# Optimization experiments

Measured on AMD Instinct MI355X. Metric: run time of the kernel, lower is better.

Reference implementation:

```python
import jax, jax.numpy as jnp
import numpy as np

B, C, H, W = 8, 384, 32, 32
NH, DK, DV = 8, 48, 48
CFF = 4 * C
L = H * W
NBIAS = (2 * H - 1) * (2 * W - 1)
LN_EPS = 1e-5


def _relative_indices(height, width):
    # rel_idx[q, k] = (gy_k - gy_q + H) * W + (gx_k - gx_q + W), matching the torch loop
    gy, gx = np.meshgrid(np.arange(height), np.arange(width), indexing='ij')
    gy = gy.ravel(); gx = gx.ravel()
    rel = (gy[None, :] - gy[:, None] + height) * width + (gx[None, :] - gx[:, None] + width)
    return jnp.asarray(rel, dtype=jnp.int64)


def setup_inputs() -> dict:
    key = jax.random.key(0)
    ks = jax.random.split(key, 10)
    s = 0.02  # small init scale
    return {
        'x': jax.random.normal(ks[0], (B, C, H, W), dtype=jnp.float32),
        'gamma': jnp.ones((C,), jnp.float32),
        'beta': jnp.zeros((C,), jnp.float32),
        'Wq': jax.random.normal(ks[1], (NH * DK, C), jnp.float32) * s,
        'Wk': jax.random.normal(ks[2], (NH * DK, C), jnp.float32) * s,
        'Wv': jax.random.normal(ks[3], (NH * DV, C), jnp.float32) * s,
        'Wo': jax.random.normal(ks[4], (C, NH * DV), jnp.float32) * s,
        'bo': jnp.zeros((C,), jnp.float32),
        'rel_bias': jax.random.normal(ks[5], (NH, NBIAS), jnp.float32),
        'fc1_w': jax.random.normal(ks[6], (CFF, C), jnp.float32) * s,
        'fc1_b': jnp.zeros((CFF,), jnp.float32),
        'fc2_w': jax.random.normal(ks[7], (C, CFF), jnp.float32) * s,
        'fc2_b': jnp.zeros((C,), jnp.float32),
        'rel_idx': _relative_indices(H, W),
    }


def reference(x, gamma, beta, Wq, Wk, Wv, Wo, bo, rel_bias,
              fc1_w, fc1_b, fc2_w, fc2_b, rel_idx):
    b, c, h_sp, w_sp = x.shape
    l = h_sp * w_sp
    nh = rel_bias.shape[0]
    dk = Wq.shape[0] // nh
    dv = Wv.shape[0] // nh

    # LayerNorm over channel dim (NHWC), then flatten to tokens [b, l, c]
    t = jnp.transpose(x, (0, 2, 3, 1))
    mu = jnp.mean(t, axis=-1, keepdims=True)
    var = jnp.mean(jnp.square(t - mu), axis=-1, keepdims=True)
    t = (t - mu) / jnp.sqrt(var + LN_EPS) * gamma + beta
    tok = t.reshape(b, l, c)

    q = (tok @ Wq.T).reshape(b, l, nh, dk)
    k = (tok @ Wk.T).reshape(b, l, nh, dk)
    v = (tok @ Wv.T).reshape(b, l, nh, dv)

    # gathered relative position bias: [nh, l, l]
    bias = rel_bias[:, rel_idx]
    # note: original applies NO 1/sqrt(d_k) scaling
    scores = jnp.einsum('blhd,bmhd->bhlm', q, k) + bias[None]
    attn = jax.nn.softmax(scores, axis=-1)
    out = jnp.einsum('bhlm,bmhd->blhd', attn, v).reshape(b, l, nh * dv)
    out = out @ Wo.T + bo  # [b, l, c]
    out = jnp.transpose(out, (0, 2, 1)).reshape(b, c, h_sp, w_sp)

    y = x + out  # attention residual (x_stem = x, no downsampling)

    # FFN: 1x1 convs == per-pixel linear over channels; exact (erf) gelu as torch default
    u = jnp.einsum('bchw,oc->bohw', y, fc1_w) + fc1_b[None, :, None, None]
    u = jax.nn.gelu(u, approximate=False)
    u = jnp.einsum('bchw,oc->bohw', u, fc2_w) + fc2_b[None, :, None, None]
    return y + u
```

## Files before the change

kernel.cpp:

```cpp
#include <hip/hip_runtime.h>
#include <math.h>

#define SL 1024
#define CH 384
#define NHEAD 8
#define DH 48
#define NBIAS 3969
#define NTOK 8192
#define BATCH 8
#define CFF 1536
#define LN_EPS 1e-5f
#define QKVLD 1152
#define HMS 3145728

#define WQKV_OFF 0
#define WO_OFF   442368
#define F1_OFF   589824
#define F2_OFF   1179648
#define WTOT     1769472

typedef float floatx4 __attribute__((ext_vector_type(4)));
typedef short bf16x8 __attribute__((ext_vector_type(8)));

__device__ __forceinline__ unsigned f2bf_u(float f) {
  unsigned u = __float_as_uint(f);
  return (u + 0x7fffu + ((u >> 16) & 1u)) >> 16;
}
__device__ __forceinline__ unsigned pack2(float a, float b) {
  return f2bf_u(a) | (f2bf_u(b) << 16);
}

__device__ __forceinline__ void gload_lds16(const void* g, void* l) {
  __builtin_amdgcn_global_load_lds(
      (const __attribute__((address_space(1))) void*)g,
      (__attribute__((address_space(3))) void*)l, 16, 0, 0);
}

__global__ void k_w2bf(const float* __restrict__ Wq, const float* __restrict__ Wk,
                       const float* __restrict__ Wv, const float* __restrict__ Wo,
                       const float* __restrict__ f1, const float* __restrict__ f2,
                       short* __restrict__ dst) {
  size_t i = ((size_t)blockIdx.x * 256 + threadIdx.x) * 8;
  if (i >= WTOT) return;
  const float* s;
  size_t base;
  if (i < 147456)        { s = Wq; base = 0; }
  else if (i < 294912)   { s = Wk; base = 147456; }
  else if (i < WO_OFF)   { s = Wv; base = 294912; }
  else if (i < F1_OFF)   { s = Wo; base = WO_OFF; }
  else if (i < F2_OFF)   { s = f1; base = F1_OFF; }
  else                   { s = f2; base = F2_OFF; }
  const float4* p = (const float4*)(s + (i - base));
  float4 a = p[0], b = p[1];
  uint4 o;
  o.x = pack2(a.x, a.y); o.y = pack2(a.z, a.w);
  o.z = pack2(b.x, b.y); o.w = pack2(b.z, b.w);
  *(uint4*)(dst + i) = o;
}

__global__ __launch_bounds__(256) void k_ln_fused(
    const float* __restrict__ x, const float* __restrict__ gamma,
    const float* __restrict__ beta, short* __restrict__ tok) {
  __shared__ float sx[32][385];
  int b = blockIdx.y, l0 = blockIdx.x * 32;
  int tid = threadIdx.x;
  const float* xb = x + (size_t)b * CH * SL;
  int cr = tid >> 3, ls = (tid & 7) * 4;
#pragma unroll
  for (int c0 = 0; c0 < CH; c0 += 32) {
    int c = c0 + cr;
    float4 v = *(const float4*)(xb + (size_t)c * SL + l0 + ls);
    sx[ls + 0][c] = v.x; sx[ls + 1][c] = v.y;
    sx[ls + 2][c] = v.z; sx[ls + 3][c] = v.w;
  }
  __syncthreads();
  int tl = tid >> 3, p = tid & 7;
  float vals[48];
  float s = 0.f, q = 0.f;
#pragma unroll
  for (int i = 0; i < 48; i++) {
    float v = sx[tl][p * 48 + i];
    vals[i] = v; s += v; q += v * v;
  }
  s += __shfl_xor(s, 1, 64); q += __shfl_xor(q, 1, 64);
  s += __shfl_xor(s, 2, 64); q += __shfl_xor(q, 2, 64);
  s += __shfl_xor(s, 4, 64); q += __shfl_xor(q, 4, 64);
  float mu = s * (1.0f / CH);
  float rstd = rsqrtf(q * (1.0f / CH) - mu * mu + LN_EPS);
  short* orow = tok + (size_t)(b * SL + l0 + tl) * CH + p * 48;
#pragma unroll
  for (int i = 0; i < 48; i += 2) {
    float a = (vals[i] - mu) * rstd * gamma[p * 48 + i] + beta[p * 48 + i];
    float c = (vals[i + 1] - mu) * rstd * gamma[p * 48 + i + 1] + beta[p * 48 + i + 1];
    *(unsigned*)(orow + i) = pack2(a, c);
  }
}

template <int BM, bool GELU, bool HAS_BIAS, int RES_MODE, int OUT_MODE>
__global__ __launch_bounds__(256) void k_gemm_mfma(
    const short* __restrict__ A, const short* __restrict__ W,
    const float* __restrict__ bias, const float* __restrict__ res,
    float* __restrict__ Cf, short* __restrict__ Cb, float* __restrict__ Ct,
    short* __restrict__ Chm, int N, int K) {
  constexpr int MI = BM / 32;
  constexpr int ASI = BM * 2 / 64;
  __shared__ short As[BM * 64];
  __shared__ short Bs[128 * 64];
  int tid = threadIdx.x;
  int wid = tid >> 6, lane = tid & 63;
  int lanelo = lane & 15, quad = lane >> 4;
  int wm = wid & 1, wn = wid >> 1;
  int m0 = blockIdx.y * BM, n0 = blockIdx.x * 128;

  const short* Aga[ASI];
  short* Ala[ASI];
#pragma unroll
  for (int s = 0; s < ASI; s++) {
    int p = wid * (BM * 2) + s * 64 + lane;
    int row = p >> 3, ch = (p & 7) ^ (row & 7);
    Aga[s] = A + (size_t)(m0 + row) * K + ch * 8;
    Ala[s] = As + (wid * (BM * 2) + s * 64) * 8;
  }
  const short* Bga[4];
  short* Bla[4];
#pragma unroll
  for (int s = 0; s < 4; s++) {
    int p = wid * 256 + s * 64 + lane;
    int row = p >> 3, ch = (p & 7) ^ (row & 7);
    Bga[s] = W + (size_t)(n0 + row) * K + ch * 8;
    Bla[s] = Bs + (wid * 256 + s * 64) * 8;
  }

  floatx4 acc[MI][4];
#pragma unroll
  for (int i = 0; i < MI; i++)
#pragma unroll
    for (int j = 0; j < 4; j++) acc[i][j] = {0.f, 0.f, 0.f, 0.f};

  int x8 = lanelo & 7;
  int ca0 = (quad ^ x8) * 8;
  int ca1 = ((quad + 4) ^ x8) * 8;

  for (int k0 = 0; k0 < K; k0 += 64) {
    __syncthreads();
#pragma unroll
    for (int s = 0; s < ASI; s++) gload_lds16(Aga[s] + k0, Ala[s]);
#pragma unroll
    for (int s = 0; s < 4; s++) gload_lds16(Bga[s] + k0, Bla[s]);
    __syncthreads();
#pragma unroll
    for (int h = 0; h < 2; h++) {
      int co = h ? ca1 : ca0;
      bf16x8 af[MI], bq[4];
#pragma unroll
      for (int i = 0; i < MI; i++)
        af[i] = *(const bf16x8*)&As[(wm * (BM / 2) + i * 16 + lanelo) * 64 + co];
#pragma unroll
      for (int j = 0; j < 4; j++)
        bq[j] = *(const bf16x8*)&Bs[(wn * 64 + j * 16 + lanelo) * 64 + co];
#pragma unroll
      for (int i = 0; i < MI; i++)
#pragma unroll
        for (int j = 0; j < 4; j++)
          acc[i][j] = __builtin_amdgcn_mfma_f32_16x16x32_bf16(af[i], bq[j], acc[i][j], 0, 0, 0);
    }
  }

  int colb = n0 + wn * 64 + lanelo;
  float bvv[4];
#pragma unroll
  for (int j = 0; j < 4; j++) bvv[j] = HAS_BIAS ? bias[colb + j * 16] : 0.0f;
#pragma unroll
  for (int i = 0; i < MI; i++) {
    int r = m0 + wm * (BM / 2) + i * 16 + quad * 4;
    int bb = r >> 10, ll = r & 1023;
#pragma unroll
    for (int j = 0; j < 4; j++) {
      int c = colb + j * 16;
      float4 rv = {0.f, 0.f, 0.f, 0.f};
      if (RES_MODE == 2) rv = *(const float4*)(res + ((size_t)bb * CH + c) * SL + ll);
      float vv[4];
#pragma unroll
      for (int reg = 0; reg < 4; reg++) {
        float v = acc[i][j][reg] + bvv[j];
        if (RES_MODE == 1) v += res[(size_t)(r + reg) * N + c];
        if (RES_MODE == 2) v += (&rv.x)[reg];
        if (GELU) v = 0.5f * v * (1.0f + erff(v * 0.7071067811865476f));
        vv[reg] = v;
      }
      if (OUT_MODE & 1) {
#pragma unroll
        for (int reg = 0; reg < 4; reg++) Cf[(size_t)(r + reg) * N + c] = vv[reg];
      }
      if (OUT_MODE & 2) {
#pragma unroll
        for (int reg = 0; reg < 4; reg++) Cb[(size_t)(r + reg) * N + c] = (short)f2bf_u(vv[reg]);
      }
      if (OUT_MODE & 4) {
        float4 ov = {vv[0], vv[1], vv[2], vv[3]};
        *(float4*)(Ct + ((size_t)bb * CH + c) * SL + ll) = ov;
      }
      if (OUT_MODE & 8) {
        int part = c / 384;
        int rem = c - part * 384;
        int hh = rem / 48, dd = rem - hh * 48;
        short* dst = Chm + (size_t)part * HMS +
                     ((size_t)(bb * NHEAD + hh) * SL + ll) * 48 + dd;
#pragma unroll
        for (int reg = 0; reg < 4; reg++) dst[reg * 48] = (short)f2bf_u(vv[reg]);
      }
    }
  }
}

__global__ __launch_bounds__(256) void k_attn_mfma(
    const short* __restrict__ qh, const short* __restrict__ kh,
    const short* __restrict__ vh, const float* __restrict__ rel_bias,
    short* __restrict__ ao) {
  __shared__ short QP[128 * 72];
  __shared__ short Ks[64 * 72];
  __shared__ short Vts[48 * 72];
  __shared__ float Bb[1152];

  int b = blockIdx.z, h = blockIdx.y;
  int l0 = blockIdx.x * 128;
  int tid = threadIdx.x;
  int wid = tid >> 6, lane = tid & 63;
  int lanelo = lane & 15, quad = lane >> 4;
  size_t hb = ((size_t)b * NHEAD + h) * SL;
  size_t bSL = (size_t)b * SL;
  const short* kbase = kh + hb * 48;
  const short* vbase = vh + hb * 48;

  {
    const short* qsrc = qh + (hb + l0) * 48;
#pragma unroll
    for (int s = 0; s < 3; s++) {
      int g = tid + 256 * s;
      int row = g / 6, pos = g - row * 6;
      *(uint4*)&QP[row * 72 + pos * 8] = *(const uint4*)(qsrc + g * 8);
    }
  }
  {
    const float* bsrc = rel_bias + h * NBIAS + (929 - l0);
    for (int j = tid; j < 1152; j += 256) Bb[j] = bsrc[j];
  }
  for (int z = tid; z < 128 * 8; z += 256) {
    int r = z >> 3, u = z & 7;
    ((unsigned*)&QP[r * 72 + 48])[u] = 0u;
    if (r < 64) ((unsigned*)&Ks[r * 72 + 48])[u] = 0u;
  }
  __syncthreads();

  bf16x8 aq[2][2];
#pragma unroll
  for (int i = 0; i < 2; i++) {
    aq[i][0] = *(const bf16x8*)&QP[(wid * 32 + i * 16 + lanelo) * 72 + quad * 8];
    aq[i][1] = *(const bf16x8*)&QP[(wid * 32 + i * 16 + lanelo) * 72 + 32 + quad * 8];
  }

  floatx4 O[2][3];
#pragma unroll
  for (int i = 0; i < 2; i++)
#pragma unroll
    for (int d = 0; d < 3; d++) O[i][d] = {0.f, 0.f, 0.f, 0.f};
  float lsum[2][4] = {{0.f, 0.f, 0.f, 0.f}, {0.f, 0.f, 0.f, 0.f}};
  int boffL[2];
#pragma unroll
  for (int i = 0; i < 2; i++)
    boffL[i] = 127 - (wid * 32 + i * 16 + quad * 4) + lanelo;

  int kg = 2 * tid;
  int krow = kg / 6, kpos = kg - krow * 6;
  int vmp = tid & 31, vdg = tid >> 5;

  short* Pw = &QP[wid * 32 * 72];

  for (int mt = 0; mt < SL; mt += 64) {
    __syncthreads();
    if (tid < 192) {
      const short* ksrc = kbase + (size_t)mt * 48 + kg * 8;
      *(uint4*)&Ks[krow * 72 + kpos * 8] = *(const uint4*)(ksrc);
      *(uint4*)&Ks[krow * 72 + (kpos + 1) * 8] = *(const uint4*)(ksrc + 8);
      const short* vs = vbase + (size_t)(mt + 2 * vmp) * 48 + vdg * 8;
      union { uint4 u; unsigned short s[8]; } va, vb;
      va.u = *(const uint4*)vs;
      vb.u = *(const uint4*)(vs + 48);
#pragma unroll
      for (int i = 0; i < 8; i++) {
        unsigned pk = (unsigned)va.s[i] | ((unsigned)vb.s[i] << 16);
        *(unsigned*)&Vts[(vdg * 8 + i) * 72 + 2 * vmp] = pk;
      }
    }
    __syncthreads();

    bf16x8 kb[4][2];
#pragma unroll
    for (int nt = 0; nt < 4; nt++) {
      kb[nt][0] = *(const bf16x8*)&Ks[(nt * 16 + lanelo) * 72 + quad * 8];
      kb[nt][1] = *(const bf16x8*)&Ks[(nt * 16 + lanelo) * 72 + 32 + quad * 8];
    }

#pragma unroll
    for (int i = 0; i < 2; i++) {
      floatx4 s[4];
#pragma unroll
      for (int nt = 0; nt < 4; nt++) {
        floatx4 a = {0.f, 0.f, 0.f, 0.f};
        a = __builtin_amdgcn_mfma_f32_16x16x32_bf16(aq[i][0], kb[nt][0], a, 0, 0, 0);
        a = __builtin_amdgcn_mfma_f32_16x16x32_bf16(aq[i][1], kb[nt][1], a, 0, 0, 0);
        s[nt] = a;
      }
#pragma unroll
      for (int nt = 0; nt < 4; nt++) {
        int mo = mt + nt * 16;
#pragma unroll
        for (int reg = 0; reg < 4; reg++) {
          float e = __expf(s[nt][reg] + Bb[boffL[i] - reg + mo]);
          lsum[i][reg] += e;
          Pw[(i * 16 + quad * 4 + reg) * 72 + nt * 16 + lanelo] = (short)f2bf_u(e);
        }
      }
    }
    __asm__ volatile("s_waitcnt lgkmcnt(0)" ::: "memory");
    bf16x8 pa[2][2];
#pragma unroll
    for (int i = 0; i < 2; i++) {
      pa[i][0] = *(const bf16x8*)&Pw[(i * 16 + lanelo) * 72 + quad * 8];
      pa[i][1] = *(const bf16x8*)&Pw[(i * 16 + lanelo) * 72 + 32 + quad * 8];
    }
#pragma unroll
    for (int d = 0; d < 3; d++) {
      bf16x8 v0 = *(const bf16x8*)&Vts[(d * 16 + lanelo) * 72 + quad * 8];
      bf16x8 v1 = *(const bf16x8*)&Vts[(d * 16 + lanelo) * 72 + 32 + quad * 8];
#pragma unroll
      for (int i = 0; i < 2; i++) {
        O[i][d] = __builtin_amdgcn_mfma_f32_16x16x32_bf16(pa[i][0], v0, O[i][d], 0, 0, 0);
        O[i][d] = __builtin_amdgcn_mfma_f32_16x16x32_bf16(pa[i][1], v1, O[i][d], 0, 0, 0);
      }
    }
  }

#pragma unroll
  for (int i = 0; i < 2; i++)
#pragma unroll
    for (int reg = 0; reg < 4; reg++) {
      float s = lsum[i][reg];
      s += __shfl_xor(s, 1, 64);
      s += __shfl_xor(s, 2, 64);
      s += __shfl_xor(s, 4, 64);
      s += __shfl_xor(s, 8, 64);
      float inv = 1.0f / s;
      size_t base =
          (bSL + (size_t)(l0 + wid * 32 + i * 16 + quad * 4 + reg)) * CH + h * DH;
      ao[base + 0 + lanelo]  = (short)f2bf_u(O[i][0][reg] * inv);
      ao[base + 16 + lanelo] = (short)f2bf_u(O[i][1][reg] * inv);
      ao[base + 32 + lanelo] = (short)f2bf_u(O[i][2][reg] * inv);
    }
}

extern "C" void kernel_launch(void* const* d_in, const int* in_sizes, int n_in,
                              void* d_out, int out_size, void* d_ws, size_t ws_size,
                              hipStream_t stream) {
  const float* x = (const float*)d_in[0];
  const float* gamma = (const float*)d_in[1];
  const float* beta = (const float*)d_in[2];
  const float* Wq = (const float*)d_in[3];
  const float* Wk = (const float*)d_in[4];
  const float* Wv = (const float*)d_in[5];
  const float* Wo = (const float*)d_in[6];
  const float* bo = (const float*)d_in[7];
  const float* rel_bias = (const float*)d_in[8];
  const float* fc1_w = (const float*)d_in[9];
  const float* fc1_b = (const float*)d_in[10];
  const float* fc2_w = (const float*)d_in[11];
  const float* fc2_b = (const float*)d_in[12];
  float* out = (float*)d_out;

  const size_t TOKCH = (size_t)NTOK * CH;
  float* ws_f = (float*)d_ws;
  float* yb = ws_f;
  short* wbf    = (short*)(yb + TOKCH);
  short* tok_bf = wbf + WTOT;
  short* hm     = tok_bf + TOKCH;
  short* ao_bf  = hm + 3 * (size_t)HMS;
  short* yb_bf  = ao_bf + TOKCH;
  short* h1_bf  = yb_bf + TOKCH;

  k_w2bf<<<WTOT / 8 / 256, 256, 0, stream>>>(Wq, Wk, Wv, Wo, fc1_w, fc2_w, wbf);
  k_ln_fused<<<dim3(SL / 32, BATCH), 256, 0, stream>>>(x, gamma, beta, tok_bf);

  k_gemm_mfma<128, false, false, 0, 8>
      <<<dim3(QKVLD / 128, NTOK / 128), 256, 0, stream>>>(
          tok_bf, wbf + WQKV_OFF, nullptr, nullptr, nullptr, nullptr, nullptr,
          hm, QKVLD, CH);

  k_attn_mfma<<<dim3(SL / 128, NHEAD, BATCH), 256, 0, stream>>>(
      hm, hm + HMS, hm + 2 * (size_t)HMS, rel_bias, ao_bf);

  k_gemm_mfma<64, false, true, 2, 3>
      <<<dim3(CH / 128, NTOK / 64), 256, 0, stream>>>(
          ao_bf, wbf + WO_OFF, bo, x, yb, yb_bf, nullptr, nullptr, CH, CH);

  k_gemm_mfma<128, true, true, 0, 2>
      <<<dim3(CFF / 128, NTOK / 128), 256, 0, stream>>>(
          yb_bf, wbf + F1_OFF, fc1_b, nullptr, nullptr, h1_bf, nullptr, nullptr,
          CFF, CH);

  k_gemm_mfma<64, false, true, 1, 4>
      <<<dim3(CH / 128, NTOK / 64), 256, 0, stream>>>(
          h1_bf, wbf + F2_OFF, fc2_b, yb, nullptr, nullptr, out, nullptr, CH, CFF);
}
```

Measured before the change: 213.6 us.

## Double-buffer GEMM LDS tiles with 32-wide K steps and compile-time K

Reworks the MFMA GEMM main loop to use two LDS buffers with a K-step of 32. The next tile's global-to-LDS load is issued before computing on the current one, so each iteration needs one barrier instead of two. K becomes a template parameter, which makes the trip count fixed at compile time, and the XOR swizzle is adapted to 4 chunks per row. The trade-off is twice as many loop iterations, each doing half the MFMA work. The async loads must also be complete before the barrier, and any latency hiding depends on how gload_lds16 waits are emitted.

```diff
diff --git a/kernel.cpp b/kernel.cpp
--- a/kernel.cpp
+++ b/kernel.cpp
@@ -96,39 +96,40 @@
   }
 }
 
-template <int BM, bool GELU, bool HAS_BIAS, int RES_MODE, int OUT_MODE>
+template <int BM, int TK, bool GELU, bool HAS_BIAS, int RES_MODE, int OUT_MODE>
 __global__ __launch_bounds__(256) void k_gemm_mfma(
     const short* __restrict__ A, const short* __restrict__ W,
     const float* __restrict__ bias, const float* __restrict__ res,
     float* __restrict__ Cf, short* __restrict__ Cb, float* __restrict__ Ct,
-    short* __restrict__ Chm, int N, int K) {
+    short* __restrict__ Chm, int N) {
+  constexpr int T = TK / 32;
   constexpr int MI = BM / 32;
-  constexpr int ASI = BM * 2 / 64;
-  __shared__ short As[BM * 64];
-  __shared__ short Bs[128 * 64];
+  constexpr int AI = BM / 64;
+  __shared__ short As[2][BM * 32];
+  __shared__ short Bs[2][128 * 32];
   int tid = threadIdx.x;
   int wid = tid >> 6, lane = tid & 63;
   int lanelo = lane & 15, quad = lane >> 4;
   int wm = wid & 1, wn = wid >> 1;
   int m0 = blockIdx.y * BM, n0 = blockIdx.x * 128;
 
-  const short* Aga[ASI];
-  short* Ala[ASI];
-#pragma unroll
-  for (int s = 0; s < ASI; s++) {
-    int p = wid * (BM * 2) + s * 64 + lane;
-    int row = p >> 3, ch = (p & 7) ^ (row & 7);
-    Aga[s] = A + (size_t)(m0 + row) * K + ch * 8;
-    Ala[s] = As + (wid * (BM * 2) + s * 64) * 8;
-  }
-  const short* Bga[4];
-  short* Bla[4];
-#pragma unroll
-  for (int s = 0; s < 4; s++) {
-    int p = wid * 256 + s * 64 + lane;
-    int row = p >> 3, ch = (p & 7) ^ (row & 7);
-    Bga[s] = W + (size_t)(n0 + row) * K + ch * 8;
-    Bla[s] = Bs + (wid * 256 + s * 64) * 8;
+  const short* Aga[AI];
+  int Alo[AI];
+#pragma unroll
+  for (int s = 0; s < AI; s++) {
+    int g = wid * (64 * AI) + s * 64 + lane;
+    int ar = g >> 2, ac = (g & 3) ^ ((g >> 3) & 3);
+    Aga[s] = A + (size_t)(m0 + ar) * TK + ac * 8;
+    Alo[s] = (wid * (64 * AI) + s * 64) * 8;
+  }
+  const short* Bga[2];
+  int Blo[2];
+#pragma unroll
+  for (int s = 0; s < 2; s++) {
+    int g = wid * 128 + s * 64 + lane;
+    int br = g >> 2, bc = (g & 3) ^ ((g >> 3) & 3);
+    Bga[s] = W + (size_t)(n0 + br) * TK + bc * 8;
+    Blo[s] = (wid * 128 + s * 64) * 8;
   }
 
   floatx4 acc[MI][4];
@@ -137,33 +138,36 @@
 #pragma unroll
     for (int j = 0; j < 4; j++) acc[i][j] = {0.f, 0.f, 0.f, 0.f};
 
-  int x8 = lanelo & 7;
-  int ca0 = (quad ^ x8) * 8;
-  int ca1 = ((quad + 4) ^ x8) * 8;
-
-  for (int k0 = 0; k0 < K; k0 += 64) {
+  int fchunk = (quad ^ ((lanelo >> 1) & 3)) * 8;
+
+#pragma unroll
+  for (int s = 0; s < AI; s++) gload_lds16(Aga[s], &As[0][Alo[s]]);
+#pragma unroll
+  for (int s = 0; s < 2; s++) gload_lds16(Bga[s], &Bs[0][Blo[s]]);
+
+  for (int t = 0; t < T; ++t) {
+    int p = t & 1;
     __syncthreads();
-#pragma unroll
-    for (int s = 0; s < ASI; s++) gload_lds16(Aga[s] + k0, Ala[s]);
-#pragma unroll
-    for (int s = 0; s < 4; s++) gload_lds16(Bga[s] + k0, Bla[s]);
-    __syncthreads();
-#pragma unroll
-    for (int h = 0; h < 2; h++) {
-      int co = h ? ca1 : ca0;
-      bf16x8 af[MI], bq[4];
-#pragma unroll
-      for (int i = 0; i < MI; i++)
-        af[i] = *(const bf16x8*)&As[(wm * (BM / 2) + i * 16 + lanelo) * 64 + co];
+    if (t + 1 < T) {
+#pragma unroll
+      for (int s = 0; s < AI; s++)
+        gload_lds16(Aga[s] + (t + 1) * 32, &As[p ^ 1][Alo[s]]);
+#pragma unroll
+      for (int s = 0; s < 2; s++)
+        gload_lds16(Bga[s] + (t + 1) * 32, &Bs[p ^ 1][Blo[s]]);
+    }
+    bf16x8 af[MI], bq[4];
+#pragma unroll
+    for (int i = 0; i < MI; i++)
+      af[i] = *(const bf16x8*)&As[p][(wm * (BM / 2) + i * 16 + lanelo) * 32 + fchunk];
+#pragma unroll
+    for (int j = 0; j < 4; j++)
+      bq[j] = *(const bf16x8*)&Bs[p][(wn * 64 + j * 16 + lanelo) * 32 + fchunk];
+#pragma unroll
+    for (int i = 0; i < MI; i++)
 #pragma unroll
       for (int j = 0; j < 4; j++)
-        bq[j] = *(const bf16x8*)&Bs[(wn * 64 + j * 16 + lanelo) * 64 + co];
-#pragma unroll
-      for (int i = 0; i < MI; i++)
-#pragma unroll
-        for (int j = 0; j < 4; j++)
-          acc[i][j] = __builtin_amdgcn_mfma_f32_16x16x32_bf16(af[i], bq[j], acc[i][j], 0, 0, 0);
-    }
+        acc[i][j] = __builtin_amdgcn_mfma_f32_16x16x32_bf16(af[i], bq[j], acc[i][j], 0, 0, 0);
   }
 
   int colb = n0 + wn * 64 + lanelo;
@@ -390,24 +394,24 @@
   k_w2bf<<<WTOT / 8 / 256, 256, 0, stream>>>(Wq, Wk, Wv, Wo, fc1_w, fc2_w, wbf);
   k_ln_fused<<<dim3(SL / 32, BATCH), 256, 0, stream>>>(x, gamma, beta, tok_bf);
 
-  k_gemm_mfma<128, false, false, 0, 8>
+  k_gemm_mfma<128, 384, false, false, 0, 8>
       <<<dim3(QKVLD / 128, NTOK / 128), 256, 0, stream>>>(
           tok_bf, wbf + WQKV_OFF, nullptr, nullptr, nullptr, nullptr, nullptr,
-          hm, QKVLD, CH);
+          hm, QKVLD);
 
   k_attn_mfma<<<dim3(SL / 128, NHEAD, BATCH), 256, 0, stream>>>(
       hm, hm + HMS, hm + 2 * (size_t)HMS, rel_bias, ao_bf);
 
-  k_gemm_mfma<64, false, true, 2, 3>
+  k_gemm_mfma<64, 384, false, true, 2, 3>
       <<<dim3(CH / 128, NTOK / 64), 256, 0, stream>>>(
-          ao_bf, wbf + WO_OFF, bo, x, yb, yb_bf, nullptr, nullptr, CH, CH);
-
-  k_gemm_mfma<128, true, true, 0, 2>
+          ao_bf, wbf + WO_OFF, bo, x, yb, yb_bf, nullptr, nullptr, CH);
+
+  k_gemm_mfma<128, 384, true, true, 0, 2>
       <<<dim3(CFF / 128, NTOK / 128), 256, 0, stream>>>(
           yb_bf, wbf + F1_OFF, fc1_b, nullptr, nullptr, h1_bf, nullptr, nullptr,
-          CFF, CH);
-
-  k_gemm_mfma<64, false, true, 1, 4>
+          CFF);
+
+  k_gemm_mfma<64, 1536, false, true, 1, 4>
       <<<dim3(CH / 128, NTOK / 64), 256, 0, stream>>>(
-          h1_bf, wbf + F2_OFF, fc2_b, yb, nullptr, nullptr, out, nullptr, CH, CFF);
-}
+          h1_bf, wbf + F2_OFF, fc2_b, yb, nullptr, nullptr, out, nullptr, CH);
+}
```

Result: slower. 220.3 us (+3.1%).

## Split attention key range in two halves with separate combine kernel

Applied to the files above, without the earlier changes.

Each attention block now processes only half of the key sequence, doubling the grid, and writes unnormalized fp32 partial outputs and row sums to workspace. A new combine kernel adds the two halves, normalizes and converts to bf16. This targets low occupancy and parallelism in the attention kernel, at the cost of extra global memory traffic for partials and an additional launch.

```diff
diff --git a/kernel.cpp b/kernel.cpp
--- a/kernel.cpp
+++ b/kernel.cpp
@@ -216,21 +216,23 @@
 __global__ __launch_bounds__(256) void k_attn_mfma(
     const short* __restrict__ qh, const short* __restrict__ kh,
     const short* __restrict__ vh, const float* __restrict__ rel_bias,
-    short* __restrict__ ao) {
+    float* __restrict__ Opart, float* __restrict__ Ls) {
   __shared__ short QP[128 * 72];
   __shared__ short Ks[64 * 72];
   __shared__ short Vts[48 * 72];
-  __shared__ float Bb[1152];
-
-  int b = blockIdx.z, h = blockIdx.y;
+  __shared__ float Bb[640];
+
+  int half = blockIdx.z & 1, b = blockIdx.z >> 1;
+  int h = blockIdx.y;
   int l0 = blockIdx.x * 128;
+  int m_lo = half * 512;
   int tid = threadIdx.x;
   int wid = tid >> 6, lane = tid & 63;
   int lanelo = lane & 15, quad = lane >> 4;
   size_t hb = ((size_t)b * NHEAD + h) * SL;
   size_t bSL = (size_t)b * SL;
-  const short* kbase = kh + hb * 48;
-  const short* vbase = vh + hb * 48;
+  const short* kbase = kh + (hb + m_lo) * 48;
+  const short* vbase = vh + (hb + m_lo) * 48;
 
   {
     const short* qsrc = qh + (hb + l0) * 48;
@@ -242,8 +244,8 @@
     }
   }
   {
-    const float* bsrc = rel_bias + h * NBIAS + (929 - l0);
-    for (int j = tid; j < 1152; j += 256) Bb[j] = bsrc[j];
+    const float* bsrc = rel_bias + h * NBIAS + (929 - l0 + m_lo);
+    for (int j = tid; j < 640; j += 256) Bb[j] = bsrc[j];
   }
   for (int z = tid; z < 128 * 8; z += 256) {
     int r = z >> 3, u = z & 7;
@@ -276,7 +278,7 @@
 
   short* Pw = &QP[wid * 32 * 72];
 
-  for (int mt = 0; mt < SL; mt += 64) {
+  for (int mt = 0; mt < 512; mt += 64) {
     __syncthreads();
     if (tid < 192) {
       const short* ksrc = kbase + (size_t)mt * 48 + kg * 8;
@@ -350,13 +352,28 @@
       s += __shfl_xor(s, 2, 64);
       s += __shfl_xor(s, 4, 64);
       s += __shfl_xor(s, 8, 64);
-      float inv = 1.0f / s;
-      size_t base =
-          (bSL + (size_t)(l0 + wid * 32 + i * 16 + quad * 4 + reg)) * CH + h * DH;
-      ao[base + 0 + lanelo]  = (short)f2bf_u(O[i][0][reg] * inv);
-      ao[base + 16 + lanelo] = (short)f2bf_u(O[i][1][reg] * inv);
-      ao[base + 32 + lanelo] = (short)f2bf_u(O[i][2][reg] * inv);
-    }
+      size_t t = bSL + (size_t)(l0 + wid * 32 + i * 16 + quad * 4 + reg);
+      float* op = Opart + ((size_t)half * NTOK + t) * CH + h * DH;
+      op[lanelo] = O[i][0][reg];
+      op[16 + lanelo] = O[i][1][reg];
+      op[32 + lanelo] = O[i][2][reg];
+      if (lanelo == 0) Ls[((size_t)half * NTOK + t) * NHEAD + h] = s;
+    }
+}
+
+__global__ __launch_bounds__(256) void k_attn_combine(
+    const float* __restrict__ Opart, const float* __restrict__ Ls,
+    short* __restrict__ ao) {
+  int gid = blockIdx.x * 256 + threadIdx.x;
+  int t = gid / 96, g = gid - t * 96;
+  int c = g * 4, h = c / DH;
+  float4 o0 = *(const float4*)(Opart + (size_t)t * CH + c);
+  float4 o1 = *(const float4*)(Opart + ((size_t)NTOK + t) * CH + c);
+  float inv = 1.0f / (Ls[(size_t)t * NHEAD + h] +
+                      Ls[((size_t)NTOK + t) * NHEAD + h]);
+  unsigned* dst = (unsigned*)(ao + (size_t)t * CH + c);
+  dst[0] = pack2((o0.x + o1.x) * inv, (o0.y + o1.y) * inv);
+  dst[1] = pack2((o0.z + o1.z) * inv, (o0.w + o1.w) * inv);
 }
 
 extern "C" void kernel_launch(void* const* d_in, const int* in_sizes, int n_in,
@@ -386,6 +403,8 @@
   short* ao_bf  = hm + 3 * (size_t)HMS;
   short* yb_bf  = ao_bf + TOKCH;
   short* h1_bf  = yb_bf + TOKCH;
+  float* Opart  = (float*)h1_bf;
+  float* Ls     = (float*)(h1_bf + (size_t)NTOK * CFF);
 
   k_w2bf<<<WTOT / 8 / 256, 256, 0, stream>>>(Wq, Wk, Wv, Wo, fc1_w, fc2_w, wbf);
   k_ln_fused<<<dim3(SL / 32, BATCH), 256, 0, stream>>>(x, gamma, beta, tok_bf);
@@ -395,8 +414,9 @@
           tok_bf, wbf + WQKV_OFF, nullptr, nullptr, nullptr, nullptr, nullptr,
           hm, QKVLD, CH);
 
-  k_attn_mfma<<<dim3(SL / 128, NHEAD, BATCH), 256, 0, stream>>>(
-      hm, hm + HMS, hm + 2 * (size_t)HMS, rel_bias, ao_bf);
+  k_attn_mfma<<<dim3(SL / 128, NHEAD, BATCH * 2), 256, 0, stream>>>(
+      hm, hm + HMS, hm + 2 * (size_t)HMS, rel_bias, Opart, Ls);
+  k_attn_combine<<<NTOK * 96 / 256, 256, 0, stream>>>(Opart, Ls, ao_bf);
 
   k_gemm_mfma<64, false, true, 2, 3>
       <<<dim3(CH / 128, NTOK / 64), 256, 0, stream>>>(
```

Result: slower. 219.2 us (+2.6%).
